# Kernel optimization log

Measured on AMD Instinct MI355X. Metric: run time of the kernel, lower is better.

The kernel has to match this reference:

```python
import jax, jax.numpy as jnp
import numpy as np

H, N2, R = 512, 16, 32   # hidden_dim, state_dim//2, dt_rank=ceil(512/16)
B, L = 1, 4096


def setup_inputs() -> dict:
    key = jax.random.key(0)
    ks = jax.random.split(key, 7)
    u = jax.random.normal(ks[0], (B, L, H), dtype=jnp.float32)
    # Parameter initialization mirroring S4DKernel.__init__
    A_log = jnp.zeros((H, N2), jnp.float32)                      # log(ones)
    A_im = jnp.broadcast_to(jnp.arange(N2, dtype=jnp.float32), (H, N2)).copy()
    B_param = jax.random.normal(ks[1], (H, N2, 2), jnp.float32)
    C_param = jax.random.normal(ks[2], (H, N2, 2), jnp.float32)
    D = jax.random.normal(ks[3], (H,), jnp.float32)
    dt_w = jax.random.normal(ks[4], (H, R), jnp.float32) / np.sqrt(R)
    dt_min, dt_max, dt_floor = 1e-3, 0.1, 1e-4
    dt_init = jnp.exp(jax.random.uniform(ks[5], (H,), jnp.float32)
                      * (np.log(dt_max) - np.log(dt_floor)) + np.log(dt_floor))
    dt_init = jnp.maximum(dt_init, dt_min)
    dt_b = dt_init + jnp.log(-jnp.expm1(-dt_init))               # inverse-softplus init
    xproj_w = jax.random.normal(ks[6], (R, H), jnp.float32) / np.sqrt(H)
    return {"u": u, "A_log": A_log, "A_im": A_im, "B_param": B_param,
            "C_param": C_param, "D": D, "dt_w": dt_w, "dt_b": dt_b,
            "xproj_w": xproj_w}


def reference(u, A_log, A_im, B_param, C_param, D, dt_w, dt_b, xproj_w):
    # Complex continuous-time parameters
    A = -jnp.exp(A_log) + 1j * A_im                 # [H, N2]
    Bc = B_param[..., 0] + 1j * B_param[..., 1]     # [H, N2]
    Cc = C_param[..., 0] + 1j * C_param[..., 1]     # [H, N2]

    # dt path: x_proj_for_dt (no bias) -> dt_proj -> softplus
    dt_u = jnp.einsum('blh,rh->blr', u, xproj_w)                    # [B,L,R]
    dt = jax.nn.softplus(jnp.einsum('blr,hr->blh', dt_u, dt_w) + dt_b)  # [B,L,H]

    # ZOH discretization
    z = dt[..., None] * A                           # [B,L,H,N2] complex
    A_bar = jnp.exp(z)
    B_bar_div = jnp.where(jnp.abs(z) < 1e-4, 1.0 + z / 2, (jnp.exp(z) - 1.0) / z)
    ub = u[..., None].astype(A_bar.dtype) * B_bar_div * Bc          # [B,L,H,N2]

    # Parallel scan for h_k = A_k * h_{k-1} + u_k (first-order linear recurrence)
    def op(c1, c2):
        a1, b1 = c1
        a2, b2 = c2
        return a1 * a2, a2 * b1 + b2
    _, h = jax.lax.associative_scan(op, (A_bar, ub), axis=1)        # [B,L,H,N2]

    y = jnp.einsum('blhn,hn->blh', h, Cc) + u * D
    return y.real
```

## Files before the change

kernel.cpp:

```cpp
#include <hip/hip_runtime.h>

#define Hd 512
#define N2d 16
#define Rd 32
#define Ld 4096
#define NCHUNK 128
#define CLEN (Ld / NCHUNK)
#define NCH (Hd * N2d)
#define NGRP 16
#define NGROUPS (NCHUNK / NGRP)

__device__ __forceinline__ bool load_consts4(const float* A_log, const float* A_im,
        const float* B_param, int hnb,
        float* Are, float* Aim, float* BAr, float* BAi) {
    #pragma unroll
    for (int j = 0; j < 4; ++j) {
        int hn = hnb + j;
        Are[j] = -__expf(A_log[hn]);
        Aim[j] = A_im[hn];
        float Bre = B_param[2 * hn];
        float Bim = B_param[2 * hn + 1];
        float inv = __builtin_amdgcn_rcpf(Are[j] * Are[j] + Aim[j] * Aim[j]);
        BAr[j] = (Bre * Are[j] + Bim * Aim[j]) * inv;
        BAi[j] = (Bim * Are[j] - Bre * Aim[j]) * inv;
    }
    float d1 = Aim[1] - Aim[0], d2 = Aim[2] - Aim[1], d3 = Aim[3] - Aim[2];
    return (Are[1] == Are[0]) && (Are[2] == Are[0]) && (Are[3] == Are[0]) &&
           (d1 == d2) && (d2 == d3);
}

__global__ __launch_bounds__(256) void k_dt(const float* __restrict__ u,
                                            const float* __restrict__ xproj_w,
                                            const float* __restrict__ dt_w,
                                            const float* __restrict__ dt_b,
                                            float2* __restrict__ du_out) {
    __shared__ float u_s[8][Hd];
    __shared__ float dtu_s[8][Rd];
    const int t = threadIdx.x;
    const int l0 = blockIdx.x * 8;

    #pragma unroll
    for (int i = 0; i < 16; ++i) {
        int idx = t + i * 256;
        ((float*)u_s)[idx] = u[l0 * Hd + idx];
    }
    __syncthreads();

    const int r = t >> 3;
    const int j = t & 7;
    float part[8];
    #pragma unroll
    for (int l = 0; l < 8; ++l) part[l] = 0.f;
    for (int k = 0; k < 64; ++k) {
        float w = xproj_w[r * Hd + k * 8 + j];
        #pragma unroll
        for (int l = 0; l < 8; ++l) part[l] = fmaf(u_s[l][k * 8 + j], w, part[l]);
    }
    #pragma unroll
    for (int off = 1; off < 8; off <<= 1) {
        #pragma unroll
        for (int l = 0; l < 8; ++l) part[l] += __shfl_xor(part[l], off);
    }
    if (j == 0) {
        #pragma unroll
        for (int l = 0; l < 8; ++l) dtu_s[l][r] = part[l];
    }
    __syncthreads();

    #pragma unroll
    for (int hb = 0; hb < 2; ++hb) {
        int h = hb * 256 + t;
        float bias = dt_b[h];
        float acc[8];
        #pragma unroll
        for (int l = 0; l < 8; ++l) acc[l] = bias;
        #pragma unroll
        for (int rb = 0; rb < 8; ++rb) {
            float4 w = *(const float4*)&dt_w[h * Rd + rb * 4];
            #pragma unroll
            for (int l = 0; l < 8; ++l) {
                acc[l] = fmaf(dtu_s[l][rb * 4 + 0], w.x, acc[l]);
                acc[l] = fmaf(dtu_s[l][rb * 4 + 1], w.y, acc[l]);
                acc[l] = fmaf(dtu_s[l][rb * 4 + 2], w.z, acc[l]);
                acc[l] = fmaf(dtu_s[l][rb * 4 + 3], w.w, acc[l]);
            }
        }
        #pragma unroll
        for (int l = 0; l < 8; ++l) {
            float x = acc[l];
            float sp = fmaxf(x, 0.f) + log1pf(__expf(-fabsf(x)));
            float uv = u_s[l][h];
            float us = uv * __builtin_amdgcn_rcpf(fmaxf(sp, 1e-30f));
            du_out[(l0 + l) * Hd + h] = make_float2(sp, us);
        }
    }
}

__global__ __launch_bounds__(256) void k_chunk(const float2* __restrict__ du,
        const float* __restrict__ A_log, const float* __restrict__ A_im,
        const float* __restrict__ B_param, const float* __restrict__ C_param,
        const float* __restrict__ Dp,
        float4* __restrict__ PS, float2* __restrict__ y1T) {
    const int t = threadIdx.x;
    const int q = t & 3;
    const int hh = blockIdx.y * 64 + (t >> 2);
    const int c = blockIdx.x;
    const int hnb = hh * N2d + q * 4;
    const int lbase = c * CLEN;

    float Are[4], Aim[4], BAr[4], BAi[4], Cre[4], Cim[4];
    const bool fast = load_consts4(A_log, A_im, B_param, hnb, Are, Aim, BAr, BAi);
    #pragma unroll
    for (int jj = 0; jj < 4; ++jj) {
        Cre[jj] = C_param[2 * (hnb + jj)];
        Cim[jj] = C_param[2 * (hnb + jj) + 1];
    }
    const float Dv = Dp[hh];

    float sr[4] = {0.f, 0.f, 0.f, 0.f}, si[4] = {0.f, 0.f, 0.f, 0.f};
    float sdt = 0.f;

    float2 b0[8], b1[8];

    #define LOADB(buf, bb)                                                     \
        { _Pragma("unroll")                                                    \
          for (int k = 0; k < 8; ++k)                                          \
              buf[k] = du[(lbase + (bb) * 8 + k) * Hd + hh]; }

    if (fast) {
        const float Are0 = Are[0], Aim0 = Aim[0], dA = Aim[1] - Aim[0];
        #define STEPF(buf, bb)                                                 \
            { _Pragma("unroll")                                                \
              for (int k = 0; k < 8; ++k) {                                    \
                int l = lbase + (bb) * 8 + k;                                  \
                float dtv = buf[k].x, us = buf[k].y;                           \
                sdt += dtv;                                                    \
                float er = __expf(dtv * Are0);                                 \
                float s0, c0, sd, cd;                                          \
                __sincosf(dtv * Aim0, &s0, &c0);                               \
                __sincosf(dtv * dA, &sd, &cd);                                 \
                float ar = er * c0, ai = er * s0;                              \
                float yv = 0.f;                                                \
                _Pragma("unroll")                                              \
                for (int jj = 0; jj < 4; ++jj) {                               \
                    float gr = fmaf(ar, us, -us);                              \
                    float gi = ai * us;                                        \
                    float nr = fmaf(ar, sr[jj], fmaf(-ai, si[jj],              \
                                 fmaf(gr, BAr[jj], -gi * BAi[jj])));           \
                    float ni = fmaf(ar, si[jj], fmaf( ai, sr[jj],              \
                                 fmaf(gr, BAi[jj],  gi * BAr[jj])));           \
                    sr[jj] = nr; si[jj] = ni;                                  \
                    yv = fmaf(nr, Cre[jj], fmaf(-ni, Cim[jj], yv));            \
                    if (jj < 3) {                                              \
                        float tr = fmaf(ar, cd, -ai * sd);                     \
                        ai = fmaf(ai, cd, ar * sd);                            \
                        ar = tr;                                               \
                    }                                                          \
                }                                                              \
                yv += __shfl_xor(yv, 1);                                       \
                yv += __shfl_xor(yv, 2);                                       \
                if (q == 0)                                                    \
                    y1T[l * Hd + hh] = make_float2(fmaf(dtv * us, Dv, yv), sdt);\
              } }
        LOADB(b0, 0);
        LOADB(b1, 1); STEPF(b0, 0);
        LOADB(b0, 2); STEPF(b1, 1);
        LOADB(b1, 3); STEPF(b0, 2);
        STEPF(b1, 3);
        #undef STEPF
    } else {
        #define STEPS(buf, bb)                                                 \
            { _Pragma("unroll")                                                \
              for (int k = 0; k < 8; ++k) {                                    \
                int l = lbase + (bb) * 8 + k;                                  \
                float dtv = buf[k].x, us = buf[k].y;                           \
                sdt += dtv;                                                    \
                float yv = 0.f;                                                \
                _Pragma("unroll")                                              \
                for (int jj = 0; jj < 4; ++jj) {                               \
                    float er = __expf(dtv * Are[jj]);                          \
                    float s, cc;                                               \
                    __sincosf(dtv * Aim[jj], &s, &cc);                         \
                    float ar = er * cc, ai = er * s;                           \
                    float gr = fmaf(ar, us, -us);                              \
                    float gi = ai * us;                                        \
                    float nr = fmaf(ar, sr[jj], fmaf(-ai, si[jj],              \
                                 fmaf(gr, BAr[jj], -gi * BAi[jj])));           \
                    float ni = fmaf(ar, si[jj], fmaf( ai, sr[jj],              \
                                 fmaf(gr, BAi[jj],  gi * BAr[jj])));           \
                    sr[jj] = nr; si[jj] = ni;                                  \
                    yv = fmaf(nr, Cre[jj], fmaf(-ni, Cim[jj], yv));            \
                }                                                              \
                yv += __shfl_xor(yv, 1);                                       \
                yv += __shfl_xor(yv, 2);                                       \
                if (q == 0)                                                    \
                    y1T[l * Hd + hh] = make_float2(fmaf(dtv * us, Dv, yv), sdt);\
              } }
        LOADB(b0, 0);
        LOADB(b1, 1); STEPS(b0, 0);
        LOADB(b0, 2); STEPS(b1, 1);
        LOADB(b1, 3); STEPS(b0, 2);
        STEPS(b1, 3);
        #undef STEPS
    }
    #undef LOADB

    int base = c * NCH + hnb;
    #pragma unroll
    for (int jj = 0; jj < 4; ++jj) {
        float er = __expf(sdt * Are[jj]);
        float s, cc;
        __sincosf(sdt * Aim[jj], &s, &cc);
        PS[base + jj] = make_float4(er * cc, er * s, sr[jj], si[jj]);
    }
}

__global__ __launch_bounds__(256) void k_group(const float4* __restrict__ PS,
                                               float4* __restrict__ IP,
                                               float4* __restrict__ Gps) {
    int idx = blockIdx.x * 256 + threadIdx.x;
    int chain = idx & (NCH - 1);
    int g = idx >> 13;
    float pr = 1.f, pi = 0.f, hr = 0.f, hi = 0.f;
    #pragma unroll
    for (int half = 0; half < 2; ++half) {
        float4 ps[8];
        #pragma unroll
        for (int i = 0; i < 8; ++i)
            ps[i] = PS[(g * NGRP + half * 8 + i) * NCH + chain];
        #pragma unroll
        for (int i = 0; i < 8; ++i) {
            int c = g * NGRP + half * 8 + i;
            IP[c * NCH + chain] = make_float4(pr, pi, hr, hi);
            float nhr = fmaf(ps[i].x, hr, fmaf(-ps[i].y, hi, ps[i].z));
            float nhi = fmaf(ps[i].x, hi, fmaf( ps[i].y, hr, ps[i].w));
            float npr = fmaf(ps[i].x, pr, -ps[i].y * pi);
            float npi = fmaf(ps[i].x, pi,  ps[i].y * pr);
            hr = nhr; hi = nhi; pr = npr; pi = npi;
        }
    }
    Gps[g * NCH + chain] = make_float4(pr, pi, hr, hi);
}

__global__ __launch_bounds__(256) void k_gscan(const float4* __restrict__ Gps,
                                               float2* __restrict__ H0g) {
    int chain = blockIdx.x * 256 + threadIdx.x;
    float4 gp[NGROUPS];
    #pragma unroll
    for (int i = 0; i < NGROUPS; ++i)
        gp[i] = Gps[i * NCH + chain];
    float hr = 0.f, hi = 0.f;
    #pragma unroll
    for (int i = 0; i < NGROUPS; ++i) {
        H0g[i * NCH + chain] = make_float2(hr, hi);
        float nr = fmaf(gp[i].x, hr, fmaf(-gp[i].y, hi, gp[i].z));
        float ni = fmaf(gp[i].x, hi, fmaf( gp[i].y, hr, gp[i].w));
        hr = nr; hi = ni;
    }
}

__global__ __launch_bounds__(256) void k_corr(const float2* __restrict__ y1T,
        const float* __restrict__ A_log, const float* __restrict__ A_im,
        const float* __restrict__ C_param, const float4* __restrict__ IP,
        const float2* __restrict__ H0g, float* __restrict__ out) {
    __shared__ float2 W_s[64][17];
    __shared__ float Ar_s[64][17];
    __shared__ float Ai_s[64][17];
    const int t = threadIdx.x;
    const int c = blockIdx.x;
    const int hg = blockIdx.y;
    const int g = c >> 4;
    const int chain0 = hg * 1024;

    #pragma unroll
    for (int i = 0; i < 4; ++i) {
        int cl = t * 4 + i;
        float4 ip = IP[c * NCH + chain0 + cl];
        float2 hgv = H0g[g * NCH + chain0 + cl];
        float h0r = fmaf(ip.x, hgv.x, fmaf(-ip.y, hgv.y, ip.z));
        float h0i = fmaf(ip.x, hgv.y, fmaf( ip.y, hgv.x, ip.w));
        float Cr = C_param[2 * (chain0 + cl)];
        float Ci = C_param[2 * (chain0 + cl) + 1];
        int hl = cl >> 4, n = cl & 15;
        W_s[hl][n] = make_float2(fmaf(Cr, h0r, -Ci * h0i),
                                 fmaf(Cr, h0i,  Ci * h0r));
        Ar_s[hl][n] = -__expf(A_log[chain0 + cl]);
        Ai_s[hl][n] = A_im[chain0 + cl];
    }
    __syncthreads();

    const int hl = t & 63;
    const int h = hg * 64 + hl;
    const int lb = t >> 6;
    const int l0 = c * CLEN + lb * 8;

    float2 yt[8];
    #pragma unroll
    for (int k = 0; k < 8; ++k) yt[k] = y1T[(l0 + k) * Hd + h];

    float2 w[N2d];
    float are[N2d], aim[N2d];
    #pragma unroll
    for (int n = 0; n < N2d; ++n) {
        w[n] = W_s[hl][n];
        are[n] = Ar_s[hl][n];
        aim[n] = Ai_s[hl][n];
    }
    float dA = aim[1] - aim[0];
    bool fast = true;
    #pragma unroll
    for (int n = 1; n < N2d; ++n)
        fast = fast && (are[n] == are[0]) && (aim[n] - aim[n - 1] == dA);

    if (fast) {
        const float Are0 = are[0], Aim0 = aim[0];
        #pragma unroll
        for (int k = 0; k < 8; ++k) {
            float T = yt[k].y;
            float er = __expf(Are0 * T);
            float s0, c0, sd, cd;
            __sincosf(Aim0 * T, &s0, &c0);
            __sincosf(dA * T, &sd, &cd);
            float ar = er * c0, ai = er * s0;
            float corr = 0.f;
            #pragma unroll
            for (int n = 0; n < N2d; ++n) {
                corr = fmaf(ar, w[n].x, fmaf(-ai, w[n].y, corr));
                if (n < N2d - 1) {
                    float tr = fmaf(ar, cd, -ai * sd);
                    ai = fmaf(ai, cd, ar * sd);
                    ar = tr;
                }
            }
            out[(l0 + k) * Hd + h] = yt[k].x + corr;
        }
    } else {
        #pragma unroll
        for (int k = 0; k < 8; ++k) {
            float T = yt[k].y;
            float corr = 0.f;
            #pragma unroll
            for (int n = 0; n < N2d; ++n) {
                float er = __expf(are[n] * T);
                float s, cc;
                __sincosf(aim[n] * T, &s, &cc);
                corr = fmaf(er * cc, w[n].x, fmaf(-er * s, w[n].y, corr));
            }
            out[(l0 + k) * Hd + h] = yt[k].x + corr;
        }
    }
}

extern "C" void kernel_launch(void* const* d_in, const int* in_sizes, int n_in,
                              void* d_out, int out_size, void* d_ws, size_t ws_size,
                              hipStream_t stream) {
    const float* u        = (const float*)d_in[0];
    const float* A_log    = (const float*)d_in[1];
    const float* A_im     = (const float*)d_in[2];
    const float* B_param  = (const float*)d_in[3];
    const float* C_param  = (const float*)d_in[4];
    const float* Dp       = (const float*)d_in[5];
    const float* dt_w     = (const float*)d_in[6];
    const float* dt_b     = (const float*)d_in[7];
    const float* xproj_w  = (const float*)d_in[8];

    float2* du  = (float2*)d_ws;
    float4* PS  = (float4*)(du + (size_t)Ld * Hd);
    float4* IP  = PS + (size_t)NCHUNK * NCH;
    float4* Gps = IP + (size_t)NCHUNK * NCH;
    float2* H0g = (float2*)(Gps + (size_t)NGROUPS * NCH);
    float2* y1T = H0g + (size_t)NGROUPS * NCH;
    float*  out = (float*)d_out;

    k_dt<<<Ld / 8, 256, 0, stream>>>(u, xproj_w, dt_w, dt_b, du);
    dim3 g2(NCHUNK, Hd / 64);
    k_chunk<<<g2, 256, 0, stream>>>(du, A_log, A_im, B_param, C_param, Dp, PS, y1T);
    k_group<<<(NCH * NGROUPS) / 256, 256, 0, stream>>>(PS, IP, Gps);
    k_gscan<<<NCH / 256, 256, 0, stream>>>(Gps, H0g);
    k_corr<<<g2, 256, 0, stream>>>(y1T, A_log, A_im, C_param, IP, H0g, out);
}
```

Measured before the change: 139.2 us.

## Fuse group scan and global scan into one kernel emitting C-weighted chunk states

Replaces the separate k_group and k_gscan kernels with a single k_comb kernel. Each block handles 32 chains across all 8 groups, combines group aggregates in shared memory, and then rescans to write the C-multiplied initial state per chunk directly. k_corr then reads those precomputed float2 W values instead of rebuilding them from IP/H0g float4 data in shared memory. This removes a kernel launch and the large IP intermediate traffic. In exchange, PS is read with strided, poorly coalesced access of 32 chains per group, and the serial cross-group loop is uneven across warps.

```diff
diff --git a/kernel.cpp b/kernel.cpp
--- a/kernel.cpp
+++ b/kernel.cpp
@@ -215,96 +215,77 @@
     }
 }
 
-__global__ __launch_bounds__(256) void k_group(const float4* __restrict__ PS,
-                                               float4* __restrict__ IP,
-                                               float4* __restrict__ Gps) {
-    int idx = blockIdx.x * 256 + threadIdx.x;
-    int chain = idx & (NCH - 1);
-    int g = idx >> 13;
+__global__ __launch_bounds__(256) void k_comb(const float4* __restrict__ PS,
+                                              const float* __restrict__ C_param,
+                                              float2* __restrict__ W) {
+    __shared__ float4 agg_s[32][NGROUPS + 1];
+    const int t = threadIdx.x;
+    const int g = t >> 5;
+    const int cl = t & 31;
+    const int chain = blockIdx.x * 32 + cl;
+
+    float4 ps[NGRP];
+    #pragma unroll
+    for (int i = 0; i < NGRP; ++i)
+        ps[i] = PS[(g * NGRP + i) * NCH + chain];
+
     float pr = 1.f, pi = 0.f, hr = 0.f, hi = 0.f;
     #pragma unroll
-    for (int half = 0; half < 2; ++half) {
-        float4 ps[8];
-        #pragma unroll
-        for (int i = 0; i < 8; ++i)
-            ps[i] = PS[(g * NGRP + half * 8 + i) * NCH + chain];
-        #pragma unroll
-        for (int i = 0; i < 8; ++i) {
-            int c = g * NGRP + half * 8 + i;
-            IP[c * NCH + chain] = make_float4(pr, pi, hr, hi);
-            float nhr = fmaf(ps[i].x, hr, fmaf(-ps[i].y, hi, ps[i].z));
-            float nhi = fmaf(ps[i].x, hi, fmaf( ps[i].y, hr, ps[i].w));
-            float npr = fmaf(ps[i].x, pr, -ps[i].y * pi);
-            float npi = fmaf(ps[i].x, pi,  ps[i].y * pr);
-            hr = nhr; hi = nhi; pr = npr; pi = npi;
-        }
-    }
-    Gps[g * NCH + chain] = make_float4(pr, pi, hr, hi);
-}
-
-__global__ __launch_bounds__(256) void k_gscan(const float4* __restrict__ Gps,
-                                               float2* __restrict__ H0g) {
-    int chain = blockIdx.x * 256 + threadIdx.x;
-    float4 gp[NGROUPS];
-    #pragma unroll
-    for (int i = 0; i < NGROUPS; ++i)
-        gp[i] = Gps[i * NCH + chain];
-    float hr = 0.f, hi = 0.f;
-    #pragma unroll
-    for (int i = 0; i < NGROUPS; ++i) {
-        H0g[i * NCH + chain] = make_float2(hr, hi);
-        float nr = fmaf(gp[i].x, hr, fmaf(-gp[i].y, hi, gp[i].z));
-        float ni = fmaf(gp[i].x, hi, fmaf( gp[i].y, hr, gp[i].w));
-        hr = nr; hi = ni;
+    for (int i = 0; i < NGRP; ++i) {
+        float nhr = fmaf(ps[i].x, hr, fmaf(-ps[i].y, hi, ps[i].z));
+        float nhi = fmaf(ps[i].x, hi, fmaf( ps[i].y, hr, ps[i].w));
+        float npr = fmaf(ps[i].x, pr, -ps[i].y * pi);
+        float npi = fmaf(ps[i].x, pi,  ps[i].y * pr);
+        hr = nhr; hi = nhi; pr = npr; pi = npi;
+    }
+    agg_s[cl][g] = make_float4(pr, pi, hr, hi);
+    __syncthreads();
+
+    float Hr = 0.f, Hi = 0.f;
+    for (int j = 0; j < g; ++j) {
+        float4 a = agg_s[cl][j];
+        float nr = fmaf(a.x, Hr, fmaf(-a.y, Hi, a.z));
+        float ni = fmaf(a.x, Hi, fmaf( a.y, Hr, a.w));
+        Hr = nr; Hi = ni;
+    }
+
+    const float Cr = C_param[2 * chain];
+    const float Ci = C_param[2 * chain + 1];
+    #pragma unroll
+    for (int i = 0; i < NGRP; ++i) {
+        int c = g * NGRP + i;
+        W[c * NCH + chain] = make_float2(fmaf(Cr, Hr, -Ci * Hi),
+                                         fmaf(Cr, Hi,  Ci * Hr));
+        float nr = fmaf(ps[i].x, Hr, fmaf(-ps[i].y, Hi, ps[i].z));
+        float ni = fmaf(ps[i].x, Hi, fmaf( ps[i].y, Hr, ps[i].w));
+        Hr = nr; Hi = ni;
     }
 }
 
 __global__ __launch_bounds__(256) void k_corr(const float2* __restrict__ y1T,
         const float* __restrict__ A_log, const float* __restrict__ A_im,
-        const float* __restrict__ C_param, const float4* __restrict__ IP,
-        const float2* __restrict__ H0g, float* __restrict__ out) {
-    __shared__ float2 W_s[64][17];
-    __shared__ float Ar_s[64][17];
-    __shared__ float Ai_s[64][17];
+        const float2* __restrict__ W, float* __restrict__ out) {
     const int t = threadIdx.x;
     const int c = blockIdx.x;
-    const int hg = blockIdx.y;
-    const int g = c >> 4;
-    const int chain0 = hg * 1024;
-
-    #pragma unroll
-    for (int i = 0; i < 4; ++i) {
-        int cl = t * 4 + i;
-        float4 ip = IP[c * NCH + chain0 + cl];
-        float2 hgv = H0g[g * NCH + chain0 + cl];
-        float h0r = fmaf(ip.x, hgv.x, fmaf(-ip.y, hgv.y, ip.z));
-        float h0i = fmaf(ip.x, hgv.y, fmaf( ip.y, hgv.x, ip.w));
-        float Cr = C_param[2 * (chain0 + cl)];
-        float Ci = C_param[2 * (chain0 + cl) + 1];
-        int hl = cl >> 4, n = cl & 15;
-        W_s[hl][n] = make_float2(fmaf(Cr, h0r, -Ci * h0i),
-                                 fmaf(Cr, h0i,  Ci * h0r));
-        Ar_s[hl][n] = -__expf(A_log[chain0 + cl]);
-        Ai_s[hl][n] = A_im[chain0 + cl];
-    }
-    __syncthreads();
-
     const int hl = t & 63;
-    const int h = hg * 64 + hl;
+    const int h = blockIdx.y * 64 + hl;
     const int lb = t >> 6;
     const int l0 = c * CLEN + lb * 8;
+    const int hn0 = h * N2d;
 
     float2 yt[8];
     #pragma unroll
     for (int k = 0; k < 8; ++k) yt[k] = y1T[(l0 + k) * Hd + h];
 
     float2 w[N2d];
+    #pragma unroll
+    for (int n = 0; n < N2d; ++n) w[n] = W[c * NCH + hn0 + n];
+
     float are[N2d], aim[N2d];
     #pragma unroll
     for (int n = 0; n < N2d; ++n) {
-        w[n] = W_s[hl][n];
-        are[n] = Ar_s[hl][n];
-        aim[n] = Ai_s[hl][n];
+        are[n] = -__expf(A_log[hn0 + n]);
+        aim[n] = A_im[hn0 + n];
     }
     float dA = aim[1] - aim[0];
     bool fast = true;
@@ -366,16 +347,13 @@
 
     float2* du  = (float2*)d_ws;
     float4* PS  = (float4*)(du + (size_t)Ld * Hd);
-    float4* IP  = PS + (size_t)NCHUNK * NCH;
-    float4* Gps = IP + (size_t)NCHUNK * NCH;
-    float2* H0g = (float2*)(Gps + (size_t)NGROUPS * NCH);
-    float2* y1T = H0g + (size_t)NGROUPS * NCH;
+    float2* W   = (float2*)(PS + (size_t)NCHUNK * NCH);
+    float2* y1T = W + (size_t)NCHUNK * NCH;
     float*  out = (float*)d_out;
 
     k_dt<<<Ld / 8, 256, 0, stream>>>(u, xproj_w, dt_w, dt_b, du);
     dim3 g2(NCHUNK, Hd / 64);
     k_chunk<<<g2, 256, 0, stream>>>(du, A_log, A_im, B_param, C_param, Dp, PS, y1T);
-    k_group<<<(NCH * NGROUPS) / 256, 256, 0, stream>>>(PS, IP, Gps);
-    k_gscan<<<NCH / 256, 256, 0, stream>>>(Gps, H0g);
-    k_corr<<<g2, 256, 0, stream>>>(y1T, A_log, A_im, C_param, IP, H0g, out);
-}
+    k_comb<<<NCH / 32, 256, 0, stream>>>(PS, C_param, W);
+    k_corr<<<g2, 256, 0, stream>>>(y1T, A_log, A_im, W, out);
+}
```

Result: faster. 134.3 us (-3.6%).
